# Kernel optimization log

Hardware: AMD Instinct MI355X
Metric: run time of the kernel (lower is better)

## Reference

```python
import jax, jax.numpy as jnp
import numpy as np

DIM = 4096
N_HEADS = 32
HEAD_DIM = DIM // N_HEADS  # 128
B = 2
S = 2048
ADAPTER_LEN = 10
NEG_INF = -1e30


def _rope(t, cos, sin):
    # t: [B, S, H, hd]; cos/sin: [S, hd//2]
    b, s, h, d = t.shape
    tr = t.reshape(b, s, h, d // 2, 2)
    a, bb = tr[..., 0], tr[..., 1]
    c = cos[None, :, None, :]
    sn = sin[None, :, None, :]
    out = jnp.stack([a * c - bb * sn, a * sn + bb * c], axis=-1)
    return out.reshape(b, s, h, d)


def _attn(q, k, v, mask=None):
    # q: [B,H,Q,d], k/v: [B,H,K,d]
    scores = jnp.einsum('bhqd,bhkd->bhqk', q, k) / np.sqrt(HEAD_DIM).astype(q.dtype)
    if mask is not None:
        scores = scores + mask
    probs = jax.nn.softmax(scores.astype(jnp.float32), axis=-1).astype(q.dtype)
    return jnp.einsum('bhqk,bhkd->bhqd', probs, v)


def setup_inputs() -> dict:
    key = jax.random.key(0)
    ks = jax.random.split(key, 8)
    w_std = 0.02
    x = jax.random.normal(ks[0], (B, S, DIM), dtype=jnp.float32)
    wq = jax.random.normal(ks[1], (DIM, DIM), dtype=jnp.float32) * w_std
    wk = jax.random.normal(ks[2], (DIM, DIM), dtype=jnp.float32) * w_std
    wv = jax.random.normal(ks[3], (DIM, DIM), dtype=jnp.float32) * w_std
    wo = jax.random.normal(ks[4], (DIM, DIM), dtype=jnp.float32) * w_std
    gate = jax.random.normal(ks[5], (1, N_HEADS, 1, 1), dtype=jnp.float32)
    adapter = jax.random.normal(ks[6], (1, ADAPTER_LEN, DIM), dtype=jnp.float32)
    # RoPE tables (theta = 10000)
    inv_freq = 1.0 / (10000.0 ** (np.arange(0, HEAD_DIM, 2, dtype=np.float32) / HEAD_DIM))
    angles = np.outer(np.arange(S, dtype=np.float32), inv_freq)  # [S, hd//2]
    freqs_cos = jnp.asarray(np.cos(angles), dtype=jnp.float32)
    freqs_sin = jnp.asarray(np.sin(angles), dtype=jnp.float32)
    # causal additive mask [1,1,S,S]
    mask = jnp.triu(jnp.full((S, S), NEG_INF, dtype=jnp.float32), k=1)[None, None]
    return {"x": x, "wq": wq, "wk": wk, "wv": wv, "wo": wo, "gate": gate,
            "adapter": adapter, "freqs_cos": freqs_cos, "freqs_sin": freqs_sin,
            "mask": mask, "start_pos": 0}


def reference(x, wq, wk, wv, wo, gate, adapter, freqs_cos, freqs_sin, mask, start_pos):
    bsz, seqlen, _ = x.shape
    # QKV projections (torch Linear: y = x @ W.T)
    xq = jnp.einsum('bsd,ed->bse', x, wq).reshape(bsz, seqlen, N_HEADS, HEAD_DIM)
    xk = jnp.einsum('bsd,ed->bse', x, wk).reshape(bsz, seqlen, N_HEADS, HEAD_DIM)
    xv = jnp.einsum('bsd,ed->bse', x, wv).reshape(bsz, seqlen, N_HEADS, HEAD_DIM)
    xq = _rope(xq, freqs_cos, freqs_sin)
    xk = _rope(xk, freqs_cos, freqs_sin)
    # KV-cache write + read: start_pos == 0 and cache is zero-initialized, so
    # keys/values over [:start_pos+seqlen] equal the freshly written xk/xv.
    q = xq.transpose(0, 2, 1, 3)      # [B,H,S,d]
    keys = xk.transpose(0, 2, 1, 3)
    values = xv.transpose(0, 2, 1, 3)
    output = _attn(q, keys, values, mask)
    # gated adapter cross-attention
    a_k = jnp.einsum('bld,ed->ble', adapter, wk).reshape(1, ADAPTER_LEN, N_HEADS, HEAD_DIM)
    a_v = jnp.einsum('bld,ed->ble', adapter, wv).reshape(1, ADAPTER_LEN, N_HEADS, HEAD_DIM)
    a_k = jnp.broadcast_to(a_k, (bsz, ADAPTER_LEN, N_HEADS, HEAD_DIM)).transpose(0, 2, 1, 3)
    a_v = jnp.broadcast_to(a_v, (bsz, ADAPTER_LEN, N_HEADS, HEAD_DIM)).transpose(0, 2, 1, 3)
    output = output + jnp.tanh(gate) * _attn(q, a_k, a_v)
    output = output.transpose(0, 2, 1, 3).reshape(bsz, seqlen, DIM)
    return jnp.einsum('bse,de->bsd', output, wo)
```

## Files before the change

### kernel.cpp

```cpp
#include <hip/hip_runtime.h>

typedef unsigned short u16;
typedef __attribute__((ext_vector_type(8))) short short8;
typedef __attribute__((ext_vector_type(4))) float f32x4;

#define L2E   1.44269504088896340736f
#define SCALE 0.08838834764831845f
#define NEGI  -1e30f
#define WN    ((size_t)4096 * 4096)
#define TNB   ((size_t)2048 * 4096)

__device__ __forceinline__ float b2f(u16 u) {
  union { float f; unsigned int i; } v; v.i = ((unsigned int)u) << 16; return v.f;
}
__device__ __forceinline__ u16 f2b(float f) {
  union { float f; unsigned int i; } v; v.f = f;
  unsigned int r = v.i + 0x7fffu + ((v.i >> 16) & 1u);
  return (u16)(r >> 16);
}
__device__ __forceinline__ void gload16(const u16* g, u16* l) {
  __builtin_amdgcn_global_load_lds((const __attribute__((address_space(1))) void*)g,
                                   (__attribute__((address_space(3))) void*)l, 16, 0, 0);
}
__device__ __forceinline__ short8 ld8_f32_to_bf16(const float* p) {
  float4 a = *(const float4*)p;
  float4 b = *(const float4*)(p + 4);
  short8 pk;
  pk[0] = (short)f2b(a.x); pk[1] = (short)f2b(a.y);
  pk[2] = (short)f2b(a.z); pk[3] = (short)f2b(a.w);
  pk[4] = (short)f2b(b.x); pk[5] = (short)f2b(b.y);
  pk[6] = (short)f2b(b.z); pk[7] = (short)f2b(b.w);
  return pk;
}

__global__ __launch_bounds__(256) void cvt_bf16(const float* __restrict__ src,
                                                u16* __restrict__ dst)
{
  size_t e = ((size_t)blockIdx.x * 256 + threadIdx.x) * 8;
  *(short8*)(dst + e) = ld8_f32_to_bf16(src + e);
}

__global__ __launch_bounds__(256, 2) void gemm_nt(const u16* __restrict__ A,
    const u16* __restrict__ B, void* __restrict__ Cv, int mode)
{
  __shared__ __align__(16) u16 As[128 * 64];
  __shared__ __align__(16) u16 Bs[128 * 64];
  const int tid  = threadIdx.x;
  const int wave = tid >> 6, lane = tid & 63;
  const int quad = lane >> 4, l16 = lane & 15;
  const int bm = blockIdx.y * 128, bn = blockIdx.x * 128;
  const int wm = (wave >> 1) * 64, wn = (wave & 1) * 64;

  f32x4 acc[4][4];
#pragma unroll
  for (int i = 0; i < 4; i++)
#pragma unroll
    for (int j = 0; j < 4; j++) acc[i][j] = (f32x4)0.0f;

  for (int k0 = 0; k0 < 4096; k0 += 64) {
    __syncthreads();
#pragma unroll
    for (int i = 0; i < 4; i++) {
      int c = tid + i * 256;
      int row = c >> 3, cb = (c & 7) << 3;
      gload16(A + (((size_t)(bm + row)) << 12) + k0 + cb, As + c * 8);
      gload16(B + (((size_t)(bn + row)) << 12) + k0 + cb, Bs + c * 8);
    }
    __syncthreads();
#pragma unroll
    for (int ks = 0; ks < 2; ks++) {
      short8 af[4], bf[4];
#pragma unroll
      for (int t = 0; t < 4; t++) {
        af[t] = *(const short8*)(As + (wm + t * 16 + l16) * 64 + ks * 32 + quad * 8);
        bf[t] = *(const short8*)(Bs + (wn + t * 16 + l16) * 64 + ks * 32 + quad * 8);
      }
#pragma unroll
      for (int mt = 0; mt < 4; mt++)
#pragma unroll
        for (int nt = 0; nt < 4; nt++)
          acc[mt][nt] = __builtin_amdgcn_mfma_f32_16x16x32_bf16(af[mt], bf[nt], acc[mt][nt], 0, 0, 0);
    }
  }
#pragma unroll
  for (int mt = 0; mt < 4; mt++)
#pragma unroll
    for (int nt = 0; nt < 4; nt++)
#pragma unroll
      for (int r = 0; r < 4; r++) {
        int row = bm + wm + mt * 16 + quad * 4 + r;
        int col = bn + wn + nt * 16 + l16;
        float v = acc[mt][nt][r];
        if (mode == 2) {
          ((float*)Cv)[(((size_t)row) << 12) + col] = v;
        } else if (mode == 1) {
          ((u16*)Cv)[((size_t)(col >> 11)) * TNB + (((size_t)row) << 11) + (col & 2047)] = f2b(v);
        } else {
          ((u16*)Cv)[(((size_t)row) << 12) + col] = f2b(v);
        }
      }
}

__global__ __launch_bounds__(256) void rope_kernel(u16* __restrict__ Q, u16* __restrict__ K,
    const float* __restrict__ fc, const float* __restrict__ fs)
{
  int gid = blockIdx.x * 256 + threadIdx.x;
  int tsel = gid >> 21;
  int r = gid & 2097151;
  int row = r >> 9, gp = r & 511;
  int s = row & 2047;
  int e0 = gp * 8;
  int i0 = (e0 >> 1) & 63;
  u16* p = (tsel ? K : Q) + (((size_t)row) << 12) + e0;
  short8 v = *(const short8*)p;
  float4 c4 = *(const float4*)(fc + s * 64 + i0);
  float4 s4 = *(const float4*)(fs + s * 64 + i0);
  float cc[4] = {c4.x, c4.y, c4.z, c4.w};
  float ss[4] = {s4.x, s4.y, s4.z, s4.w};
  short8 w;
#pragma unroll
  for (int j = 0; j < 4; j++) {
    float a  = b2f((u16)v[2 * j]);
    float bb = b2f((u16)v[2 * j + 1]);
    w[2 * j]     = (short)f2b(a * cc[j] - bb * ss[j]);
    w[2 * j + 1] = (short)f2b(a * ss[j] + bb * cc[j]);
  }
  *(short8*)p = w;
}

__global__ __launch_bounds__(256) void adapter_kv(const float* __restrict__ adapter,
    const float* __restrict__ wk, const float* __restrict__ wv,
    u16* __restrict__ ak, u16* __restrict__ av)
{
  int gid  = blockIdx.x * 4 + (threadIdx.x >> 6);
  int lane = threadIdx.x & 63;
  int which = (gid >= 40960) ? 1 : 0;
  int rem = gid - which * 40960;
  int l = rem >> 12, col = rem & 4095;
  const float* w = which ? wv : wk;
  u16* o = which ? av : ak;
  const float* arow = adapter + l * 4096;
  const float* wrow = w + (((size_t)col) << 12);
  float sum = 0.f;
#pragma unroll
  for (int i = 0; i < 8; i++) {
    int e = i * 512 + lane * 8;
    float4 a0 = *(const float4*)(arow + e);
    float4 a1 = *(const float4*)(arow + e + 4);
    float4 w0 = *(const float4*)(wrow + e);
    float4 w1 = *(const float4*)(wrow + e + 4);
    sum += a0.x * w0.x + a0.y * w0.y + a0.z * w0.z + a0.w * w0.w
         + a1.x * w1.x + a1.y * w1.y + a1.z * w1.z + a1.w * w1.w;
  }
#pragma unroll
  for (int off = 1; off < 64; off <<= 1) sum += __shfl_xor(sum, off, 64);
  if (lane == 0) o[rem] = f2b(sum);
}

__global__ __launch_bounds__(256, 2) void flash_attn(const u16* __restrict__ Q,
    const u16* __restrict__ K, const u16* __restrict__ V, u16* __restrict__ O)
{
  Q += (size_t)blockIdx.z * TNB;
  K += (size_t)blockIdx.z * TNB;
  V += (size_t)blockIdx.z * TNB;
  O += (size_t)blockIdx.z * TNB;
  __shared__ __align__(16) u16 sm[24576];
  u16* Ks = sm;
  u16* Vs = sm + 8192;
  u16* Ps = sm + 16384;
  const int tid  = threadIdx.x;
  const int wave = tid >> 6, lane = tid & 63;
  const int quad = lane >> 4, l16 = lane & 15;
  const int qt = blockIdx.x;
  const int h  = blockIdx.y;
  const int q0 = qt * 128;
  const size_t qkBase = (size_t)h * 128;
  const size_t vBase  = ((size_t)(h * 128)) << 11;

#pragma unroll
  for (int i = 0; i < 8; i++) {
    int c = tid + i * 256;
    int row = c >> 4;
    int cb  = ((c & 15) ^ (row & 7)) << 3;
    gload16(Q + qkBase + (((size_t)(q0 + row)) << 12) + cb, sm + c * 8);
  }
  __syncthreads();
  short8 qa[2][4];
#pragma unroll
  for (int mt = 0; mt < 2; mt++)
#pragma unroll
    for (int ks = 0; ks < 4; ks++) {
      int qr = wave * 32 + mt * 16 + l16;
      qa[mt][ks] = *(const short8*)(sm + qr * 128 + (((ks * 4 + quad) ^ (qr & 7)) << 3));
    }

  f32x4 acc_o[2][8];
#pragma unroll
  for (int mt = 0; mt < 2; mt++)
#pragma unroll
    for (int n = 0; n < 8; n++) acc_o[mt][n] = (f32x4)0.0f;
  float m_st[2][4], l_st[2][4];
#pragma unroll
  for (int mt = 0; mt < 2; mt++)
#pragma unroll
    for (int r = 0; r < 4; r++) { m_st[mt][r] = NEGI; l_st[mt][r] = 0.f; }

  const int qw0 = q0 + wave * 32;
  const int ntiles = 2 * (qt + 1);
  for (int t = 0; t < ntiles; t++) {
    const int kv0 = t * 64;
    __syncthreads();
#pragma unroll
    for (int i = 0; i < 4; i++) {
      int c = tid + i * 256;
      int krow = c >> 4;
      int kcb  = ((c & 15) ^ (krow & 7)) << 3;
      gload16(K + qkBase + (((size_t)(kv0 + krow)) << 12) + kcb, Ks + c * 8);
      int vrow = c >> 3;
      int vcb  = ((c & 7) ^ (vrow & 7)) << 3;
      gload16(V + vBase + (((size_t)vrow) << 11) + kv0 + vcb, Vs + c * 8);
    }
    __syncthreads();

    if (kv0 <= qw0 + 31) {
      f32x4 sc[2][4];
#pragma unroll
      for (int mt = 0; mt < 2; mt++)
#pragma unroll
        for (int nt = 0; nt < 4; nt++) sc[mt][nt] = (f32x4)0.0f;
      __builtin_amdgcn_s_setprio(1);
#pragma unroll
      for (int ks = 0; ks < 4; ks++) {
        short8 kb[4];
#pragma unroll
        for (int nt = 0; nt < 4; nt++) {
          int kr = nt * 16 + l16;
          kb[nt] = *(const short8*)(Ks + kr * 128 + (((ks * 4 + quad) ^ (kr & 7)) << 3));
        }
#pragma unroll
        for (int mt = 0; mt < 2; mt++)
#pragma unroll
          for (int nt = 0; nt < 4; nt++)
            sc[mt][nt] = __builtin_amdgcn_mfma_f32_16x16x32_bf16(qa[mt][ks], kb[nt], sc[mt][nt], 0, 0, 0);
      }
      __builtin_amdgcn_s_setprio(0);
#pragma unroll
      for (int mt = 0; mt < 2; mt++)
#pragma unroll
        for (int nt = 0; nt < 4; nt++)
#pragma unroll
          for (int r = 0; r < 4; r++) {
            int qrow = qw0 + mt * 16 + quad * 4 + r;
            int key  = kv0 + nt * 16 + l16;
            float s = sc[mt][nt][r] * SCALE;
            sc[mt][nt][r] = (key > qrow) ? NEGI : s;
          }
      float alpha[2][4];
#pragma unroll
      for (int mt = 0; mt < 2; mt++)
#pragma unroll
        for (int r = 0; r < 4; r++) {
          float mx = fmaxf(fmaxf(sc[mt][0][r], sc[mt][1][r]), fmaxf(sc[mt][2][r], sc[mt][3][r]));
          mx = fmaxf(mx, __shfl_xor(mx, 1, 64));
          mx = fmaxf(mx, __shfl_xor(mx, 2, 64));
          mx = fmaxf(mx, __shfl_xor(mx, 4, 64));
          mx = fmaxf(mx, __shfl_xor(mx, 8, 64));
          float mnew = fmaxf(m_st[mt][r], mx);
          float al = __builtin_amdgcn_exp2f((m_st[mt][r] - mnew) * L2E);
          float rs = 0.f;
#pragma unroll
          for (int nt = 0; nt < 4; nt++) {
            float p = __builtin_amdgcn_exp2f((sc[mt][nt][r] - mnew) * L2E);
            sc[mt][nt][r] = p;
            rs += p;
          }
          rs += __shfl_xor(rs, 1, 64);
          rs += __shfl_xor(rs, 2, 64);
          rs += __shfl_xor(rs, 4, 64);
          rs += __shfl_xor(rs, 8, 64);
          l_st[mt][r] = l_st[mt][r] * al + rs;
          m_st[mt][r] = mnew;
          alpha[mt][r] = al;
        }
#pragma unroll
      for (int mt = 0; mt < 2; mt++)
#pragma unroll
        for (int n = 0; n < 8; n++)
#pragma unroll
          for (int r = 0; r < 4; r++) acc_o[mt][n][r] *= alpha[mt][r];
      u16* Pw = Ps + wave * 2048;
#pragma unroll
      for (int mt = 0; mt < 2; mt++)
#pragma unroll
        for (int nt = 0; nt < 4; nt++)
#pragma unroll
          for (int r = 0; r < 4; r++) {
            int prow = mt * 16 + quad * 4 + r;
            int pcol = nt * 16 + l16;
            Pw[prow * 64 + (((pcol >> 3) ^ (prow & 7)) << 3) + (pcol & 7)] = f2b(sc[mt][nt][r]);
          }
      __builtin_amdgcn_s_setprio(1);
#pragma unroll
      for (int ks2 = 0; ks2 < 2; ks2++) {
        short8 pa[2];
#pragma unroll
        for (int mt = 0; mt < 2; mt++) {
          int pr = mt * 16 + l16;
          pa[mt] = *(const short8*)(Pw + pr * 64 + (((ks2 * 4 + quad) ^ (pr & 7)) << 3));
        }
#pragma unroll
        for (int n = 0; n < 8; n++) {
          int vr = n * 16 + l16;
          short8 vb = *(const short8*)(Vs + vr * 64 + (((ks2 * 4 + quad) ^ (vr & 7)) << 3));
#pragma unroll
          for (int mt = 0; mt < 2; mt++)
            acc_o[mt][n] = __builtin_amdgcn_mfma_f32_16x16x32_bf16(pa[mt], vb, acc_o[mt][n], 0, 0, 0);
        }
      }
      __builtin_amdgcn_s_setprio(0);
    }
  }
#pragma unroll
  for (int mt = 0; mt < 2; mt++)
#pragma unroll
    for (int r = 0; r < 4; r++) {
      float inv = 1.0f / l_st[mt][r];
      int qrow = qw0 + mt * 16 + quad * 4 + r;
#pragma unroll
      for (int n = 0; n < 8; n++) {
        int d = n * 16 + l16;
        O[qkBase + (((size_t)qrow) << 12) + d] = f2b(acc_o[mt][n][r] * inv);
      }
    }
}

__global__ __launch_bounds__(256) void adapter_attn(const u16* __restrict__ Q,
    const u16* __restrict__ ak, const u16* __restrict__ av,
    const float* __restrict__ gate, u16* __restrict__ AO)
{
  int gid  = blockIdx.x * 4 + (threadIdx.x >> 6);
  int lane = threadIdx.x & 63;
  int row = gid >> 5, h = gid & 31;
  float g = tanhf(gate[h]);
  const u16* qp = Q + (((size_t)row) << 12) + h * 128 + lane * 2;
  float qa = b2f(qp[0]), qb = b2f(qp[1]);
  float p[10];
#pragma unroll
  for (int l = 0; l < 10; l++) {
    const u16* kp = ak + l * 4096 + h * 128 + lane * 2;
    p[l] = qa * b2f(kp[0]) + qb * b2f(kp[1]);
  }
#pragma unroll
  for (int l = 0; l < 10; l++)
#pragma unroll
    for (int off = 1; off < 64; off <<= 1) p[l] += __shfl_xor(p[l], off, 64);
  float m = NEGI;
#pragma unroll
  for (int l = 0; l < 10; l++) { p[l] *= SCALE; m = fmaxf(m, p[l]); }
  float sum = 0.f;
#pragma unroll
  for (int l = 0; l < 10; l++) { p[l] = __builtin_amdgcn_exp2f((p[l] - m) * L2E); sum += p[l]; }
  float gi = g / sum;
  float a0 = 0.f, a1 = 0.f;
#pragma unroll
  for (int l = 0; l < 10; l++) {
    const u16* vp = av + l * 4096 + h * 128 + lane * 2;
    a0 += p[l] * b2f(vp[0]);
    a1 += p[l] * b2f(vp[1]);
  }
  u16* op = AO + (((size_t)row) << 12) + h * 128 + lane * 2;
  op[0] = f2b(b2f(op[0]) + gi * a0);
  op[1] = f2b(b2f(op[1]) + gi * a1);
}

extern "C" void kernel_launch(void* const* d_in, const int* in_sizes, int n_in,
                              void* d_out, int out_size, void* d_ws, size_t ws_size,
                              hipStream_t stream) {
  (void)in_sizes; (void)n_in; (void)out_size; (void)ws_size;
  const float* x       = (const float*)d_in[0];
  const float* wq      = (const float*)d_in[1];
  const float* wk      = (const float*)d_in[2];
  const float* wv      = (const float*)d_in[3];
  const float* wo      = (const float*)d_in[4];
  const float* gate    = (const float*)d_in[5];
  const float* adapter = (const float*)d_in[6];
  const float* fc      = (const float*)d_in[7];
  const float* fs      = (const float*)d_in[8];
  float* out = (float*)d_out;

  u16* wb  = (u16*)d_ws;
  u16* xb  = wb + WN;
  u16* Qf  = xb + WN;
  u16* Kf  = Qf + WN;
  u16* Vtf = Kf + WN;
  u16* AOf = xb;
  u16* ak  = Vtf + WN;
  u16* av  = ak + 40960;

  adapter_kv<<<20480, 256, 0, stream>>>(adapter, wk, wv, ak, av);
  cvt_bf16<<<8192, 256, 0, stream>>>(x, xb);

  cvt_bf16<<<8192, 256, 0, stream>>>(wq, wb);
  gemm_nt<<<dim3(32, 32), 256, 0, stream>>>(xb, wb, Qf, 0);
  cvt_bf16<<<8192, 256, 0, stream>>>(wk, wb);
  gemm_nt<<<dim3(32, 32), 256, 0, stream>>>(xb, wb, Kf, 0);
  cvt_bf16<<<8192, 256, 0, stream>>>(wv, wb);
  gemm_nt<<<dim3(32, 32), 256, 0, stream>>>(wb, xb, Vtf, 1);

  rope_kernel<<<16384, 256, 0, stream>>>(Qf, Kf, fc, fs);
  flash_attn<<<dim3(16, 32, 2), 256, 0, stream>>>(Qf, Kf, Vtf, AOf);
  adapter_attn<<<32768, 256, 0, stream>>>(Qf, ak, av, gate, AOf);

  cvt_bf16<<<8192, 256, 0, stream>>>(wo, wb);
  gemm_nt<<<dim3(32, 32), 256, 0, stream>>>(AOf, wb, out, 2);
}
```

Before: 1.612 ms.

## Double-buffer K/V tiles in flash attention and schedule heaviest query tiles first

The flash attention kernel now prefetches the next K/V tile into a second LDS buffer while the current tile is computed, with a single barrier per iteration instead of two. The grid is reordered so heads and batch vary fastest and query tiles run in reverse order, which puts the longest causal blocks at the start for better load balance. LDS use per block rises from 48KB to 80KB, which may limit how many blocks fit on a CU despite the launch bound of 2.

```diff
diff --git a/kernel.cpp b/kernel.cpp
--- a/kernel.cpp
+++ b/kernel.cpp
@@ -160,29 +160,38 @@
 __global__ __launch_bounds__(256, 2) void flash_attn(const u16* __restrict__ Q,
     const u16* __restrict__ K, const u16* __restrict__ V, u16* __restrict__ O)
 {
-  Q += (size_t)blockIdx.z * TNB;
-  K += (size_t)blockIdx.z * TNB;
-  V += (size_t)blockIdx.z * TNB;
-  O += (size_t)blockIdx.z * TNB;
-  __shared__ __align__(16) u16 sm[24576];
-  u16* Ks = sm;
-  u16* Vs = sm + 8192;
-  u16* Ps = sm + 16384;
+  Q += (size_t)blockIdx.y * TNB;
+  K += (size_t)blockIdx.y * TNB;
+  V += (size_t)blockIdx.y * TNB;
+  O += (size_t)blockIdx.y * TNB;
+  __shared__ __align__(16) u16 sm[40960];
+  u16* Ps = sm + 32768;
   const int tid  = threadIdx.x;
   const int wave = tid >> 6, lane = tid & 63;
   const int quad = lane >> 4, l16 = lane & 15;
-  const int qt = blockIdx.x;
-  const int h  = blockIdx.y;
+  const int qt = 15 - blockIdx.z;
+  const int h  = blockIdx.x;
   const int q0 = qt * 128;
   const size_t qkBase = (size_t)h * 128;
   const size_t vBase  = ((size_t)(h * 128)) << 11;
 
+  u16* Qs = sm + 16384;
 #pragma unroll
   for (int i = 0; i < 8; i++) {
     int c = tid + i * 256;
     int row = c >> 4;
     int cb  = ((c & 15) ^ (row & 7)) << 3;
-    gload16(Q + qkBase + (((size_t)(q0 + row)) << 12) + cb, sm + c * 8);
+    gload16(Q + qkBase + (((size_t)(q0 + row)) << 12) + cb, Qs + c * 8);
+  }
+#pragma unroll
+  for (int i = 0; i < 4; i++) {
+    int c = tid + i * 256;
+    int krow = c >> 4;
+    int kcb  = ((c & 15) ^ (krow & 7)) << 3;
+    gload16(K + qkBase + (((size_t)krow) << 12) + kcb, sm + c * 8);
+    int vrow = c >> 3;
+    int vcb  = ((c & 7) ^ (vrow & 7)) << 3;
+    gload16(V + vBase + (((size_t)vrow) << 11) + vcb, sm + 8192 + c * 8);
   }
   __syncthreads();
   short8 qa[2][4];
@@ -191,8 +200,9 @@
 #pragma unroll
     for (int ks = 0; ks < 4; ks++) {
       int qr = wave * 32 + mt * 16 + l16;
-      qa[mt][ks] = *(const short8*)(sm + qr * 128 + (((ks * 4 + quad) ^ (qr & 7)) << 3));
-    }
+      qa[mt][ks] = *(const short8*)(Qs + qr * 128 + (((ks * 4 + quad) ^ (qr & 7)) << 3));
+    }
+  __syncthreads();
 
   f32x4 acc_o[2][8];
 #pragma unroll
@@ -209,18 +219,23 @@
   const int ntiles = 2 * (qt + 1);
   for (int t = 0; t < ntiles; t++) {
     const int kv0 = t * 64;
-    __syncthreads();
-#pragma unroll
-    for (int i = 0; i < 4; i++) {
-      int c = tid + i * 256;
-      int krow = c >> 4;
-      int kcb  = ((c & 15) ^ (krow & 7)) << 3;
-      gload16(K + qkBase + (((size_t)(kv0 + krow)) << 12) + kcb, Ks + c * 8);
-      int vrow = c >> 3;
-      int vcb  = ((c & 7) ^ (vrow & 7)) << 3;
-      gload16(V + vBase + (((size_t)vrow) << 11) + kv0 + vcb, Vs + c * 8);
-    }
-    __syncthreads();
+    u16* Kc = sm + (t & 1) * 16384;
+    u16* Vc = Kc + 8192;
+    if (t + 1 < ntiles) {
+      const int nk = kv0 + 64;
+      u16* Kn = sm + ((t + 1) & 1) * 16384;
+      u16* Vn = Kn + 8192;
+#pragma unroll
+      for (int i = 0; i < 4; i++) {
+        int c = tid + i * 256;
+        int krow = c >> 4;
+        int kcb  = ((c & 15) ^ (krow & 7)) << 3;
+        gload16(K + qkBase + (((size_t)(nk + krow)) << 12) + kcb, Kn + c * 8);
+        int vrow = c >> 3;
+        int vcb  = ((c & 7) ^ (vrow & 7)) << 3;
+        gload16(V + vBase + (((size_t)vrow) << 11) + nk + vcb, Vn + c * 8);
+      }
+    }
 
     if (kv0 <= qw0 + 31) {
       f32x4 sc[2][4];
@@ -235,7 +250,7 @@
 #pragma unroll
         for (int nt = 0; nt < 4; nt++) {
           int kr = nt * 16 + l16;
-          kb[nt] = *(const short8*)(Ks + kr * 128 + (((ks * 4 + quad) ^ (kr & 7)) << 3));
+          kb[nt] = *(const short8*)(Kc + kr * 128 + (((ks * 4 + quad) ^ (kr & 7)) << 3));
         }
 #pragma unroll
         for (int mt = 0; mt < 2; mt++)
@@ -311,7 +326,7 @@
 #pragma unroll
         for (int n = 0; n < 8; n++) {
           int vr = n * 16 + l16;
-          short8 vb = *(const short8*)(Vs + vr * 64 + (((ks2 * 4 + quad) ^ (vr & 7)) << 3));
+          short8 vb = *(const short8*)(Vc + vr * 64 + (((ks2 * 4 + quad) ^ (vr & 7)) << 3));
 #pragma unroll
           for (int mt = 0; mt < 2; mt++)
             acc_o[mt][n] = __builtin_amdgcn_mfma_f32_16x16x32_bf16(pa[mt], vb, acc_o[mt][n], 0, 0, 0);
@@ -319,6 +334,7 @@
       }
       __builtin_amdgcn_s_setprio(0);
     }
+    __syncthreads();
   }
 #pragma unroll
   for (int mt = 0; mt < 2; mt++)
@@ -408,7 +424,7 @@
   gemm_nt<<<dim3(32, 32), 256, 0, stream>>>(wb, xb, Vtf, 1);
 
   rope_kernel<<<16384, 256, 0, stream>>>(Qf, Kf, fc, fs);
-  flash_attn<<<dim3(16, 32, 2), 256, 0, stream>>>(Qf, Kf, Vtf, AOf);
+  flash_attn<<<dim3(32, 2, 16), 256, 0, stream>>>(Qf, Kf, Vtf, AOf);
   adapter_attn<<<32768, 256, 0, stream>>>(Qf, ak, av, gate, AOf);
 
   cvt_bf16<<<8192, 256, 0, stream>>>(wo, wb);
```

After: 1.488 ms. 7.7% less time.
